# Optimization experiments

Measured on AMD Instinct MI355X. Metric: run time of the kernel, lower is better.

The kernel has to match this reference:

```python
import jax, jax.numpy as jnp
import numpy as np


def _conv1x1(x, w, b):
    # x: (B,C,H,W), w: (O,C), b: (O,)
    return jnp.einsum('oc,bchw->bohw', w, x) + b[None, :, None, None]


def _avg_pool2(x):
    B, C, H, W = x.shape
    return x.reshape(B, C, H // 2, 2, W // 2, 2).mean(axis=(3, 5))


def setup_inputs() -> dict:
    key = jax.random.key(0)
    B, C, H, W = 8, 64, 64, 64
    ks = jax.random.split(key, 14)
    s = 1.0 / np.sqrt(C)

    def wb(k1, k2):
        return (jax.random.uniform(k1, (C, C), jnp.float32, -s, s),
                jax.random.uniform(k2, (C,), jnp.float32, -s, s))

    w_q, b_q = wb(ks[0], ks[1])
    w_K, b_K = wb(ks[2], ks[3])
    w_V, b_V = wb(ks[4], ks[5])
    w_Q, b_Q = wb(ks[6], ks[7])
    w_k, b_k = wb(ks[8], ks[9])
    w_v, b_v = wb(ks[10], ks[11])
    x = jax.random.normal(ks[12], (B, C, H, W), jnp.float32)
    gamma = jnp.ones((1,), jnp.float32)
    return dict(x=x, w_q=w_q, b_q=b_q, w_K=w_K, b_K=b_K, w_V=w_V, b_V=b_V,
                w_Q=w_Q, b_Q=b_Q, w_k=w_k, b_k=b_k, w_v=w_v, b_v=b_v,
                gamma=gamma)


def reference(x, w_q, b_q, w_K, b_K, w_V, b_V, w_Q, b_Q, w_k, b_k, w_v, b_v, gamma):
    B, C, H, W = x.shape
    N = H * W
    N4 = N // 4

    # Stage 1: pooled queries vs full key/value
    q = _conv1x1(x, w_q, b_q)                      # (B,C,H,W); torch views as (B,C,W,H) but H==W
    qp = _avg_pool2(q).reshape(B, C, N4).transpose(0, 2, 1)   # (B,N/4,C)
    Kf = _conv1x1(x, w_K, b_K).reshape(B, C, N)                # (B,C,N)
    Vf = _conv1x1(x, w_V, b_V).reshape(B, C, N)                # (B,C,N)
    attn = jax.nn.softmax(jnp.einsum('bnc,bcm->bnm', qp, Kf), axis=-1)  # (B,N/4,N)
    out = jnp.einsum('bcm,bnm->bcn', Vf, attn)                 # (B,C,N/4)
    out = out.reshape(B, C, H // 2, W // 2)

    # Stage 2: full queries vs pooled-derived key/value
    Qf = _conv1x1(x, w_Q, b_Q).reshape(B, C, N).transpose(0, 2, 1)  # (B,N,C)
    kp = _conv1x1(out, w_k, b_k).reshape(B, C, N4)                  # (B,C,N/4)
    vp = _conv1x1(out, w_v, b_v).reshape(B, C, N4)                  # (B,C,N/4)
    attn2 = jax.nn.softmax(jnp.einsum('bnc,bcm->bnm', Qf, kp), axis=-1)  # (B,N,N/4)
    out2 = jnp.einsum('bcm,bnm->bcn', vp, attn2).reshape(B, C, H, W)

    return gamma * out2 + x
```

## Files before the change

kernel.cpp:

```cpp
#include <hip/hip_runtime.h>
#include <math.h>


typedef __bf16 bf16;
typedef __attribute__((ext_vector_type(4))) __bf16 bf16x4;
typedef __attribute__((ext_vector_type(8))) __bf16 bf16x8;
typedef __attribute__((ext_vector_type(4))) float f32x4;

__device__ __forceinline__ void proj_wave(
    const bf16* __restrict__ src, int TN,
    const float* __restrict__ W, const float* __restrict__ Bs,
    bf16* __restrict__ Y, int tr, int N, int b, int gn0, int lane)
{
    const int c16 = lane & 15, q4 = lane >> 4;
    bf16x8 wa[4][2];
    #pragma unroll
    for (int to = 0; to < 4; ++to)
        #pragma unroll
        for (int h = 0; h < 2; ++h) {
            const float* wp = W + (16 * to + c16) * 64 + q4 * 8 + 32 * h;
            float4 f0 = *(const float4*)wp;
            float4 f1 = *(const float4*)(wp + 4);
            bf16 tmp[8] = {(bf16)f0.x, (bf16)f0.y, (bf16)f0.z, (bf16)f0.w,
                           (bf16)f1.x, (bf16)f1.y, (bf16)f1.z, (bf16)f1.w};
            wa[to][h] = *(bf16x8*)tmp;
        }
    for (int tn = 0; tn < TN; ++tn) {
        bf16x8 xb0 = *(const bf16x8*)&src[(16 * tn + c16) * 72 + q4 * 8];
        bf16x8 xb1 = *(const bf16x8*)&src[(16 * tn + c16) * 72 + q4 * 8 + 32];
        #pragma unroll
        for (int to = 0; to < 4; ++to) {
            f32x4 acc = (f32x4){0.f, 0.f, 0.f, 0.f};
            acc = __builtin_amdgcn_mfma_f32_16x16x32_bf16(wa[to][0], xb0, acc, 0, 0, 0);
            acc = __builtin_amdgcn_mfma_f32_16x16x32_bf16(wa[to][1], xb1, acc, 0, 0, 0);
            if (tr) {
                float4 b4 = *(const float4*)(Bs + 16 * to + q4 * 4);
                bf16x4 yv;
                yv[0] = (bf16)(acc[0] + b4.x); yv[1] = (bf16)(acc[1] + b4.y);
                yv[2] = (bf16)(acc[2] + b4.z); yv[3] = (bf16)(acc[3] + b4.w);
                *(bf16x4*)(Y + ((size_t)b * N + gn0 + 16 * tn + c16) * 64 + 16 * to + q4 * 4) = yv;
            } else {
                float4 b4 = *(const float4*)(Bs + 16 * to + q4 * 4);
                float bias[4] = {b4.x, b4.y, b4.z, b4.w};
                #pragma unroll
                for (int r = 0; r < 4; ++r)
                    Y[((size_t)b * 64 + 16 * to + q4 * 4 + r) * N + gn0 + 16 * tn + c16] =
                        (bf16)(acc[r] + bias[r]);
            }
        }
    }
}

__global__ __launch_bounds__(256) void prep_kernel(
    const float* __restrict__ x,
    const float* __restrict__ w_K, const float* __restrict__ b_K, bf16* __restrict__ Kt,
    const float* __restrict__ w_Q, const float* __restrict__ b_Q, bf16* __restrict__ Qt,
    const float* __restrict__ w_V, const float* __restrict__ b_V, bf16* __restrict__ Vf,
    const float* __restrict__ w_q, const float* __restrict__ b_q, bf16* __restrict__ qpt)
{
    __shared__ float tile[128 * 65];
    __shared__ __align__(16) bf16 xbT[128 * 72];
    __shared__ __align__(16) bf16 xpb[32 * 72];
    const int t  = threadIdx.x;
    const int h2 = blockIdx.x;
    const int b  = blockIdx.y;
    const int n0 = h2 * 128;

    #pragma unroll
    for (int i = 0; i < 32; ++i) {
        int lin = i * 256 + t;
        int n = lin & 127, c = lin >> 7;
        tile[n * 65 + c] = x[((size_t)b * 64 + c) * 4096 + n0 + n];
    }
    __syncthreads();
    #pragma unroll
    for (int i = 0; i < 4; ++i) {
        int slot = i * 256 + t;
        int n = slot >> 3, c0 = (slot & 7) * 8;
        bf16 tmp[8];
        #pragma unroll
        for (int j = 0; j < 8; ++j) tmp[j] = (bf16)tile[n * 65 + c0 + j];
        *(bf16x8*)&xbT[n * 72 + c0] = *(bf16x8*)tmp;
    }
    {
        int wp = t & 31, c0 = (t >> 5) * 8;
        bf16 tmp[8];
        #pragma unroll
        for (int j = 0; j < 8; ++j) {
            float a = tile[(2 * wp) * 65 + c0 + j] + tile[(2 * wp + 1) * 65 + c0 + j]
                    + tile[(64 + 2 * wp) * 65 + c0 + j] + tile[(64 + 2 * wp + 1) * 65 + c0 + j];
            tmp[j] = (bf16)(0.25f * a);
        }
        *(bf16x8*)&xpb[wp * 72 + c0] = *(bf16x8*)tmp;
    }
    __syncthreads();

    const int lane = t & 63;
    const int w    = t >> 6;
    {
        const int mat  = w >> 1;
        const int half = w & 1;
        proj_wave(xbT + half * 64 * 72, 4,
                  mat == 0 ? w_K : w_Q, mat == 0 ? b_K : b_Q,
                  mat == 0 ? Kt : Qt, 1, 4096, b, n0 + half * 64, lane);
    }
    if (w < 2) {
        proj_wave(xbT + w * 64 * 72, 4, w_V, b_V, Vf, 0, 4096, b, n0 + w * 64, lane);
    } else if (w == 2) {
        proj_wave(xpb, 2, w_q, b_q, qpt, 1, 1024, b, h2 * 32, lane);
    }
}

template<int NSPLIT, int PLAYOUT>
__global__ __launch_bounds__(256) void flash_kernel(
    const bf16* __restrict__ Qt, const bf16* __restrict__ Kt,
    const bf16* __restrict__ Vn, int NQ, int L,
    bf16* __restrict__ Opart, float* __restrict__ Mbuf, float* __restrict__ Lbuf)
{
    const int tid  = threadIdx.x;
    const int lane = tid & 63;
    const int w    = tid >> 6;
    const int c16  = lane & 15;
    const int q4   = lane >> 4;
    const int b    = blockIdx.y;
    const int n0   = blockIdx.x * 128 + w * 32;
    const int s    = blockIdx.z;
    const int SL   = L / NSPLIT;
    const int k0   = s * SL;
    const int ntiles = SL / 64;

    __shared__ __align__(16) bf16 Ks[2][64 * 72];
    __shared__ __align__(16) bf16 Vs[2][64 * 72];
    __shared__ __align__(16) bf16 Pw[4][32 * 72];

    const int srow = tid >> 2;
    const int scol = (tid & 3) * 16;

    const bf16* Kb = Kt + (size_t)b * L * 64;
    const bf16* Vb = Vn + (size_t)b * 64 * L;

    bf16x8 bq[2][2];
    #pragma unroll
    for (int u = 0; u < 2; ++u) {
        const bf16* qrow = Qt + ((size_t)b * NQ + n0 + 16 * u + c16) * 64 + q4 * 8;
        bq[u][0] = *(const bf16x8*)(qrow);
        bq[u][1] = *(const bf16x8*)(qrow + 32);
    }

    f32x4 O[2][4];
    #pragma unroll
    for (int u = 0; u < 2; ++u)
        #pragma unroll
        for (int g = 0; g < 4; ++g) O[u][g] = (f32x4){0.f, 0.f, 0.f, 0.f};
    float m_run[2] = {-INFINITY, -INFINITY};
    float l_run[2] = {0.f, 0.f};

    {
        const bf16* kg = Kb + ((size_t)(k0 + srow)) * 64 + scol;
        *(bf16x8*)&Ks[0][srow * 72 + scol]     = *(const bf16x8*)kg;
        *(bf16x8*)&Ks[0][srow * 72 + scol + 8] = *(const bf16x8*)(kg + 8);
        const bf16* vg = Vb + (size_t)srow * L + k0 + scol;
        *(bf16x8*)&Vs[0][srow * 72 + scol]     = *(const bf16x8*)vg;
        *(bf16x8*)&Vs[0][srow * 72 + scol + 8] = *(const bf16x8*)(vg + 8);
    }
    __syncthreads();

    for (int it = 0; it < ntiles; ++it) {
        const int buf = it & 1;
        if (it + 1 < ntiles) {
            const int kn = k0 + (it + 1) * 64;
            const bf16* kg = Kb + ((size_t)(kn + srow)) * 64 + scol;
            *(bf16x8*)&Ks[buf ^ 1][srow * 72 + scol]     = *(const bf16x8*)kg;
            *(bf16x8*)&Ks[buf ^ 1][srow * 72 + scol + 8] = *(const bf16x8*)(kg + 8);
            const bf16* vg = Vb + (size_t)srow * L + kn + scol;
            *(bf16x8*)&Vs[buf ^ 1][srow * 72 + scol]     = *(const bf16x8*)vg;
            *(bf16x8*)&Vs[buf ^ 1][srow * 72 + scol + 8] = *(const bf16x8*)(vg + 8);
        }

        f32x4 sv[2][4];
        #pragma unroll
        for (int t = 0; t < 4; ++t) {
            const bf16* krow = &Ks[buf][(16 * t + c16) * 72 + q4 * 8];
            bf16x8 ak0 = *(const bf16x8*)(krow);
            bf16x8 ak1 = *(const bf16x8*)(krow + 32);
            #pragma unroll
            for (int u = 0; u < 2; ++u) {
                f32x4 z = (f32x4){0.f, 0.f, 0.f, 0.f};
                z = __builtin_amdgcn_mfma_f32_16x16x32_bf16(ak0, bq[u][0], z, 0, 0, 0);
                sv[u][t] = __builtin_amdgcn_mfma_f32_16x16x32_bf16(ak1, bq[u][1], z, 0, 0, 0);
            }
        }

        #pragma unroll
        for (int u = 0; u < 2; ++u) {
            float mx = sv[u][0][0];
            #pragma unroll
            for (int t = 0; t < 4; ++t)
                #pragma unroll
                for (int r = 0; r < 4; ++r) mx = fmaxf(mx, sv[u][t][r]);
            mx = fmaxf(mx, __shfl_xor(mx, 16));
            mx = fmaxf(mx, __shfl_xor(mx, 32));
            float nm = fmaxf(m_run[u], mx);
            float alpha = __expf(m_run[u] - nm);
            m_run[u] = nm;

            float ls = 0.f;
            #pragma unroll
            for (int t = 0; t < 4; ++t)
                #pragma unroll
                for (int r = 0; r < 4; ++r) {
                    float p = __expf(sv[u][t][r] - nm);
                    sv[u][t][r] = p;
                    ls += p;
                }
            ls += __shfl_xor(ls, 16);
            ls += __shfl_xor(ls, 32);
            l_run[u] = l_run[u] * alpha + ls;
            #pragma unroll
            for (int g = 0; g < 4; ++g)
                #pragma unroll
                for (int r = 0; r < 4; ++r) O[u][g][r] *= alpha;

            #pragma unroll
            for (int t = 0; t < 4; ++t) {
                bf16x4 pv;
                pv[0] = (bf16)sv[u][t][0]; pv[1] = (bf16)sv[u][t][1];
                pv[2] = (bf16)sv[u][t][2]; pv[3] = (bf16)sv[u][t][3];
                *(bf16x4*)&Pw[w][(16 * u + c16) * 72 + 16 * t + 4 * q4] = pv;
            }
        }

        #pragma unroll
        for (int h = 0; h < 2; ++h) {
            bf16x8 pf0 = *(const bf16x8*)&Pw[w][(c16) * 72 + 32 * h + 8 * q4];
            bf16x8 pf1 = *(const bf16x8*)&Pw[w][(16 + c16) * 72 + 32 * h + 8 * q4];
            #pragma unroll
            for (int g = 0; g < 4; ++g) {
                bf16x8 av = *(const bf16x8*)&Vs[buf][(16 * g + c16) * 72 + 32 * h + q4 * 8];
                O[0][g] = __builtin_amdgcn_mfma_f32_16x16x32_bf16(av, pf0, O[0][g], 0, 0, 0);
                O[1][g] = __builtin_amdgcn_mfma_f32_16x16x32_bf16(av, pf1, O[1][g], 0, 0, 0);
            }
        }
        __syncthreads();
    }

    #pragma unroll
    for (int u = 0; u < 2; ++u) {
        float inv = 1.0f / l_run[u];
        if (PLAYOUT == 1) {
            bf16* dst = Opart + ((size_t)(b * NSPLIT + s) * NQ + n0 + 16 * u + c16) * 64 + q4 * 4;
            #pragma unroll
            for (int g = 0; g < 4; ++g) {
                bf16x4 yv;
                #pragma unroll
                for (int r = 0; r < 4; ++r) yv[r] = (bf16)(O[u][g][r] * inv);
                *(bf16x4*)(dst + 16 * g) = yv;
            }
        } else {
            #pragma unroll
            for (int g = 0; g < 4; ++g)
                #pragma unroll
                for (int r = 0; r < 4; ++r)
                    Opart[((size_t)(b * NSPLIT + s) * 64 + 16 * g + 4 * q4 + r) * NQ + n0 + 16 * u + c16] =
                        (bf16)(O[u][g][r] * inv);
        }
    }
    if (lane < 16) {
        #pragma unroll
        for (int u = 0; u < 2; ++u) {
            Mbuf[(b * NSPLIT + s) * NQ + n0 + 16 * u + lane] = m_run[u];
            Lbuf[(b * NSPLIT + s) * NQ + n0 + 16 * u + lane] = l_run[u];
        }
    }
}

__global__ __launch_bounds__(256) void comb1kv_kernel(
    const bf16* __restrict__ Opart, const float* __restrict__ Mbuf,
    const float* __restrict__ Lbuf,
    const float* __restrict__ w_k, const float* __restrict__ b_k, bf16* __restrict__ kpt,
    const float* __restrict__ w_v, const float* __restrict__ b_v, bf16* __restrict__ vp)
{
    __shared__ __align__(16) bf16 tile[32 * 72];
    __shared__ float wbuf[32 * 8];
    const int t  = threadIdx.x;
    const int m0 = blockIdx.x * 32;
    const int b  = blockIdx.y;

    if (t < 32) {
        int m = m0 + t;
        float ms[8], ls[8];
        #pragma unroll
        for (int s = 0; s < 8; ++s) {
            ms[s] = Mbuf[(b * 8 + s) * 1024 + m];
            ls[s] = Lbuf[(b * 8 + s) * 1024 + m];
        }
        float M = ms[0];
        #pragma unroll
        for (int s = 1; s < 8; ++s) M = fmaxf(M, ms[s]);
        float wsv[8], lt = 0.f;
        #pragma unroll
        for (int s = 0; s < 8; ++s) { wsv[s] = ls[s] * __expf(ms[s] - M); lt += wsv[s]; }
        float inv = 1.f / lt;
        #pragma unroll
        for (int s = 0; s < 8; ++s) wbuf[t * 8 + s] = wsv[s] * inv;
    }
    __syncthreads();

    #pragma unroll
    for (int i = 0; i < 2; ++i) {
        int ml = i * 16 + (t >> 4);
        int c4 = (t & 15) * 4;
        const bf16* base = Opart + ((size_t)(b * 8) * 1024 + m0 + ml) * 64 + c4;
        float a0 = 0.f, a1 = 0.f, a2 = 0.f, a3 = 0.f;
        #pragma unroll
        for (int s = 0; s < 8; ++s) {
            bf16x4 v = *(const bf16x4*)(base + (size_t)s * 1024 * 64);
            float wg = wbuf[ml * 8 + s];
            a0 += (float)v[0] * wg; a1 += (float)v[1] * wg;
            a2 += (float)v[2] * wg; a3 += (float)v[3] * wg;
        }
        bf16x4 o; o[0] = (bf16)a0; o[1] = (bf16)a1; o[2] = (bf16)a2; o[3] = (bf16)a3;
        *(bf16x4*)&tile[ml * 72 + c4] = o;
    }
    __syncthreads();

    const int lane = t & 63;
    const int w    = t >> 6;
    const int c16 = lane & 15, q4 = lane >> 4;

    if (w < 2) {
        bf16x8 wb[4][2];
        #pragma unroll
        for (int to = 0; to < 4; ++to)
            #pragma unroll
            for (int h = 0; h < 2; ++h) {
                const float* wp = w_k + (16 * to + c16) * 64 + q4 * 8 + 32 * h;
                float4 f0 = *(const float4*)wp;
                float4 f1 = *(const float4*)(wp + 4);
                bf16 tmp[8] = {(bf16)f0.x, (bf16)f0.y, (bf16)f0.z, (bf16)f0.w,
                               (bf16)f1.x, (bf16)f1.y, (bf16)f1.z, (bf16)f1.w};
                wb[to][h] = *(bf16x8*)tmp;
            }
        const int tm = w;
        bf16x8 a0 = *(const bf16x8*)&tile[(16 * tm + c16) * 72 + q4 * 8];
        bf16x8 a1 = *(const bf16x8*)&tile[(16 * tm + c16) * 72 + q4 * 8 + 32];
        #pragma unroll
        for (int to = 0; to < 4; ++to) {
            f32x4 acc = (f32x4){0.f, 0.f, 0.f, 0.f};
            acc = __builtin_amdgcn_mfma_f32_16x16x32_bf16(a0, wb[to][0], acc, 0, 0, 0);
            acc = __builtin_amdgcn_mfma_f32_16x16x32_bf16(a1, wb[to][1], acc, 0, 0, 0);
            float bias = b_k[16 * to + c16];
            #pragma unroll
            for (int r = 0; r < 4; ++r)
                kpt[((size_t)b * 1024 + m0 + 16 * tm + 4 * q4 + r) * 64 + 16 * to + c16] =
                    (bf16)(acc[r] + bias);
        }
    } else {
        bf16x8 wa[4][2];
        #pragma unroll
        for (int ta = 0; ta < 4; ++ta)
            #pragma unroll
            for (int h = 0; h < 2; ++h) {
                const float* wp = w_v + (16 * ta + c16) * 64 + q4 * 8 + 32 * h;
                float4 f0 = *(const float4*)wp;
                float4 f1 = *(const float4*)(wp + 4);
                bf16 tmp[8] = {(bf16)f0.x, (bf16)f0.y, (bf16)f0.z, (bf16)f0.w,
                               (bf16)f1.x, (bf16)f1.y, (bf16)f1.z, (bf16)f1.w};
                wa[ta][h] = *(bf16x8*)tmp;
            }
        const int tm = w - 2;
        bf16x8 bb0 = *(const bf16x8*)&tile[(16 * tm + c16) * 72 + q4 * 8];
        bf16x8 bb1 = *(const bf16x8*)&tile[(16 * tm + c16) * 72 + q4 * 8 + 32];
        #pragma unroll
        for (int ta = 0; ta < 4; ++ta) {
            f32x4 acc = (f32x4){0.f, 0.f, 0.f, 0.f};
            acc = __builtin_amdgcn_mfma_f32_16x16x32_bf16(wa[ta][0], bb0, acc, 0, 0, 0);
            acc = __builtin_amdgcn_mfma_f32_16x16x32_bf16(wa[ta][1], bb1, acc, 0, 0, 0);
            float4 b4 = *(const float4*)(b_v + 16 * ta + 4 * q4);
            float bias[4] = {b4.x, b4.y, b4.z, b4.w};
            #pragma unroll
            for (int r = 0; r < 4; ++r)
                vp[((size_t)b * 64 + 16 * ta + 4 * q4 + r) * 1024 + m0 + 16 * tm + c16] =
                    (bf16)(acc[r] + bias[r]);
        }
    }
}

__global__ __launch_bounds__(256) void combine2_kernel(
    const bf16* __restrict__ Opart, const float* __restrict__ Mbuf,
    const float* __restrict__ Lbuf, const float* __restrict__ x,
    const float* __restrict__ gamma_p, float* __restrict__ out)
{
    int idx = blockIdx.x * 256 + threadIdx.x;
    int n = idx & 4095;
    int b = idx >> 18;
    int c = (idx >> 12) & 63;
    float m0 = Mbuf[(b * 2 + 0) * 4096 + n], m1 = Mbuf[(b * 2 + 1) * 4096 + n];
    float l0 = Lbuf[(b * 2 + 0) * 4096 + n], l1 = Lbuf[(b * 2 + 1) * 4096 + n];
    float M = fmaxf(m0, m1);
    float w0 = l0 * __expf(m0 - M), w1 = l1 * __expf(m1 - M);
    float acc = (float)Opart[((size_t)(b * 2 + 0) * 64 + c) * 4096 + n] * w0
              + (float)Opart[((size_t)(b * 2 + 1) * 64 + c) * 4096 + n] * w1;
    out[idx] = gamma_p[0] * (acc / (w0 + w1)) + x[idx];
}

extern "C" void kernel_launch(void* const* d_in, const int* in_sizes, int n_in,
                              void* d_out, int out_size, void* d_ws, size_t ws_size,
                              hipStream_t stream) {
    const float* x    = (const float*)d_in[0];
    const float* w_q  = (const float*)d_in[1];
    const float* b_q  = (const float*)d_in[2];
    const float* w_K  = (const float*)d_in[3];
    const float* b_K  = (const float*)d_in[4];
    const float* w_V  = (const float*)d_in[5];
    const float* b_V  = (const float*)d_in[6];
    const float* w_Q  = (const float*)d_in[7];
    const float* b_Q  = (const float*)d_in[8];
    const float* w_k  = (const float*)d_in[9];
    const float* b_k  = (const float*)d_in[10];
    const float* w_v  = (const float*)d_in[11];
    const float* b_v  = (const float*)d_in[12];
    const float* gamma = (const float*)d_in[13];
    float* out = (float*)d_out;

    char* ws = (char*)d_ws;
    bf16*  Kt    = (bf16*)ws;   ws += (size_t)8 * 4096 * 64 * 2;
    bf16*  Qt    = (bf16*)ws;   ws += (size_t)8 * 4096 * 64 * 2;
    bf16*  Vf    = (bf16*)ws;   ws += (size_t)8 * 4096 * 64 * 2;
    bf16*  qpt   = (bf16*)ws;   ws += (size_t)8 * 1024 * 64 * 2;
    bf16*  kpt   = (bf16*)ws;   ws += (size_t)8 * 1024 * 64 * 2;
    bf16*  vp    = (bf16*)ws;   ws += (size_t)8 * 64 * 1024 * 2;
    bf16*  Opart = (bf16*)ws;   ws += (size_t)8 * 8 * 1024 * 64 * 2;
    float* Mb    = (float*)ws;  ws += (size_t)8 * 8 * 1024 * 4;
    float* Lb    = (float*)ws;  ws += (size_t)8 * 8 * 1024 * 4;

    prep_kernel<<<dim3(32, 8), 256, 0, stream>>>(
        x, w_K, b_K, Kt, w_Q, b_Q, Qt, w_V, b_V, Vf, w_q, b_q, qpt);

    flash_kernel<8, 1><<<dim3(8, 8, 8), 256, 0, stream>>>(
        qpt, Kt, Vf, 1024, 4096, Opart, Mb, Lb);

    comb1kv_kernel<<<dim3(32, 8), 256, 0, stream>>>(
        Opart, Mb, Lb, w_k, b_k, kpt, w_v, b_v, vp);

    flash_kernel<2, 0><<<dim3(32, 8, 2), 256, 0, stream>>>(
        Qt, kpt, vp, 4096, 1024, Opart, Mb, Lb);

    combine2_kernel<<<8192, 256, 0, stream>>>(Opart, Mb, Lb, x, gamma, out);
}
```

Baseline: 150.2 us.

## Load K/V tiles directly to LDS with swizzled unpadded layout

Replaces the register-staged global-to-LDS copies of the K and V tiles in the flash kernel with global_load_lds direct transfers. The padded stride-72 layout becomes a stride-64 layout with an XOR-style rotation swizzle so MFMA fragment reads avoid bank conflicts. It also adds an occupancy hint of 3 blocks per CU to launch_bounds. The intent is to cut VGPR staging and instruction overhead in the load path. The risk is that the asynchronous loads are not waited on explicitly beyond __syncthreads, which depends on the compiler inserting the correct vmcnt waits.

```diff
diff --git a/kernel.cpp b/kernel.cpp
--- a/kernel.cpp
+++ b/kernel.cpp
@@ -6,6 +6,13 @@
 typedef __attribute__((ext_vector_type(4))) __bf16 bf16x4;
 typedef __attribute__((ext_vector_type(8))) __bf16 bf16x8;
 typedef __attribute__((ext_vector_type(4))) float f32x4;
+
+__device__ __forceinline__ void gl_lds16(const bf16* g, bf16* l) {
+    __builtin_amdgcn_global_load_lds(
+        (const __attribute__((address_space(1))) unsigned int*)g,
+        (__attribute__((address_space(3))) unsigned int*)l,
+        16, 0, 0);
+}
 
 __device__ __forceinline__ void proj_wave(
     const bf16* __restrict__ src, int TN,
@@ -112,7 +119,7 @@
 }
 
 template<int NSPLIT, int PLAYOUT>
-__global__ __launch_bounds__(256) void flash_kernel(
+__global__ __launch_bounds__(256, 3) void flash_kernel(
     const bf16* __restrict__ Qt, const bf16* __restrict__ Kt,
     const bf16* __restrict__ Vn, int NQ, int L,
     bf16* __restrict__ Opart, float* __restrict__ Mbuf, float* __restrict__ Lbuf)
@@ -129,12 +136,12 @@
     const int k0   = s * SL;
     const int ntiles = SL / 64;
 
-    __shared__ __align__(16) bf16 Ks[2][64 * 72];
-    __shared__ __align__(16) bf16 Vs[2][64 * 72];
+    __shared__ __align__(16) bf16 Ks[2][64 * 64];
+    __shared__ __align__(16) bf16 Vs[2][64 * 64];
     __shared__ __align__(16) bf16 Pw[4][32 * 72];
 
-    const int srow = tid >> 2;
-    const int scol = (tid & 3) * 16;
+    const int rl8 = lane >> 3;
+    const int cg  = ((lane & 7) - rl8) & 7;
 
     const bf16* Kb = Kt + (size_t)b * L * 64;
     const bf16* Vb = Vn + (size_t)b * 64 * L;
@@ -155,13 +162,11 @@
     float m_run[2] = {-INFINITY, -INFINITY};
     float l_run[2] = {0.f, 0.f};
 
-    {
-        const bf16* kg = Kb + ((size_t)(k0 + srow)) * 64 + scol;
-        *(bf16x8*)&Ks[0][srow * 72 + scol]     = *(const bf16x8*)kg;
-        *(bf16x8*)&Ks[0][srow * 72 + scol + 8] = *(const bf16x8*)(kg + 8);
-        const bf16* vg = Vb + (size_t)srow * L + k0 + scol;
-        *(bf16x8*)&Vs[0][srow * 72 + scol]     = *(const bf16x8*)vg;
-        *(bf16x8*)&Vs[0][srow * 72 + scol + 8] = *(const bf16x8*)(vg + 8);
+    #pragma unroll
+    for (int j = 0; j < 2; ++j) {
+        const int row = 16 * w + 8 * j + rl8;
+        gl_lds16(Kb + (size_t)(k0 + row) * 64 + cg * 8, &Ks[0][(16 * w + 8 * j) * 64]);
+        gl_lds16(Vb + (size_t)row * L + k0 + cg * 8,    &Vs[0][(16 * w + 8 * j) * 64]);
     }
     __syncthreads();
 
@@ -169,20 +174,20 @@
         const int buf = it & 1;
         if (it + 1 < ntiles) {
             const int kn = k0 + (it + 1) * 64;
-            const bf16* kg = Kb + ((size_t)(kn + srow)) * 64 + scol;
-            *(bf16x8*)&Ks[buf ^ 1][srow * 72 + scol]     = *(const bf16x8*)kg;
-            *(bf16x8*)&Ks[buf ^ 1][srow * 72 + scol + 8] = *(const bf16x8*)(kg + 8);
-            const bf16* vg = Vb + (size_t)srow * L + kn + scol;
-            *(bf16x8*)&Vs[buf ^ 1][srow * 72 + scol]     = *(const bf16x8*)vg;
-            *(bf16x8*)&Vs[buf ^ 1][srow * 72 + scol + 8] = *(const bf16x8*)(vg + 8);
+            #pragma unroll
+            for (int j = 0; j < 2; ++j) {
+                const int row = 16 * w + 8 * j + rl8;
+                gl_lds16(Kb + (size_t)(kn + row) * 64 + cg * 8, &Ks[buf ^ 1][(16 * w + 8 * j) * 64]);
+                gl_lds16(Vb + (size_t)row * L + kn + cg * 8,    &Vs[buf ^ 1][(16 * w + 8 * j) * 64]);
+            }
         }
 
         f32x4 sv[2][4];
         #pragma unroll
         for (int t = 0; t < 4; ++t) {
-            const bf16* krow = &Ks[buf][(16 * t + c16) * 72 + q4 * 8];
-            bf16x8 ak0 = *(const bf16x8*)(krow);
-            bf16x8 ak1 = *(const bf16x8*)(krow + 32);
+            const bf16* krow = &Ks[buf][(16 * t + c16) * 64];
+            bf16x8 ak0 = *(const bf16x8*)&krow[((q4 + c16) & 7) * 8];
+            bf16x8 ak1 = *(const bf16x8*)&krow[((q4 + 4 + c16) & 7) * 8];
             #pragma unroll
             for (int u = 0; u < 2; ++u) {
                 f32x4 z = (f32x4){0.f, 0.f, 0.f, 0.f};
@@ -236,7 +241,7 @@
             bf16x8 pf1 = *(const bf16x8*)&Pw[w][(16 + c16) * 72 + 32 * h + 8 * q4];
             #pragma unroll
             for (int g = 0; g < 4; ++g) {
-                bf16x8 av = *(const bf16x8*)&Vs[buf][(16 * g + c16) * 72 + 32 * h + q4 * 8];
+                bf16x8 av = *(const bf16x8*)&Vs[buf][(16 * g + c16) * 64 + ((4 * h + q4 + c16) & 7) * 8];
                 O[0][g] = __builtin_amdgcn_mfma_f32_16x16x32_bf16(av, pf0, O[0][g], 0, 0, 0);
                 O[1][g] = __builtin_amdgcn_mfma_f32_16x16x32_bf16(av, pf1, O[1][g], 0, 0, 0);
             }
```

Result: no change. 149.3 us (-0.6%).
